# Optimization experiments

Hardware: AMD Instinct MI355X
Metric: run time of the kernel (lower is better)

## Reference

```python
import jax, jax.numpy as jnp
import numpy as np

N_NODES = 100000
N_EDGES = 1600000
DK = 32
OUT_DIM = 32


def setup_inputs() -> dict:
    key = jax.random.key(0)
    ks = jax.random.split(key, 7)
    X = jax.random.normal(ks[0], (N_NODES, DK), dtype=jnp.float32)
    K = jax.random.normal(ks[1], (N_NODES, DK), dtype=jnp.float32)
    V = jax.random.normal(ks[2], (N_NODES, DK), dtype=jnp.float32)
    # output projection (nn.Dense(out_dim)) params
    W_o = jax.random.normal(ks[3], (DK, OUT_DIM), dtype=jnp.float32) / np.sqrt(DK)
    b_o = jnp.zeros((OUT_DIM,), dtype=jnp.float32)
    # sparsity descriptor td: edge list, dst sorted so segment ops see sorted ids
    src = jax.random.randint(ks[4], (N_EDGES,), 0, N_NODES, dtype=jnp.int32)
    dst = jnp.sort(jax.random.randint(ks[5], (N_EDGES,), 0, N_NODES, dtype=jnp.int32))
    return {"X": X, "K": K, "V": V, "W_o": W_o, "b_o": b_o,
            "src": src, "dst": dst, "num_seg": N_NODES}


def reference(X, K, V, W_o, b_o, src, dst, num_seg):
    dk = X.shape[-1]
    # per-edge attention logits: <Q[dst], K[src]> / dk  -> (E,)
    scores = jnp.einsum('ed,ed->e', jnp.take(X, dst, axis=0),
                        jnp.take(K, src, axis=0)) / dk
    # segment (per-neighborhood) softmax over edges sharing a dst node
    seg_max = jax.ops.segment_max(scores, dst, num_segments=num_seg,
                                  indices_are_sorted=True)
    e = jnp.exp(scores - jnp.take(seg_max, dst))
    denom = jax.ops.segment_sum(e, dst, num_segments=num_seg,
                                indices_are_sorted=True)
    alpha = e / jnp.take(denom, dst)  # (E,)
    # weighted aggregation of values, scattered back to nodes -> (N, dk)
    agg = jax.ops.segment_sum(alpha[:, None] * jnp.take(V, src, axis=0), dst,
                              num_segments=num_seg, indices_are_sorted=True)
    # output projection W_o
    return agg @ W_o + b_o
```

## Files before the change

kernel.cpp:

```cpp
#include <hip/hip_runtime.h>
#include <math.h>

#define DK 32
#define OUT_DIM 32

typedef float    f32x4 __attribute__((ext_vector_type(4)));
typedef _Float16 h2    __attribute__((ext_vector_type(2)));
typedef _Float16 h8    __attribute__((ext_vector_type(8)));

#if __has_builtin(__builtin_amdgcn_fdot2)
#define FDOT2(a, b, c) __builtin_amdgcn_fdot2((a), (b), (c), false)
#else
#define FDOT2(a, b, c) ((c) + (float)(a).x * (float)(b).x + (float)(a).y * (float)(b).y)
#endif

#if __has_builtin(__builtin_amdgcn_exp2f)
#define EXP2F(x) __builtin_amdgcn_exp2f(x)
#else
#define EXP2F(x) exp2f(x)
#endif

__device__ __forceinline__ h2 as_h2(unsigned u) {
    union { unsigned u; h2 h; } v; v.u = u; return v.h;
}
__device__ __forceinline__ unsigned as_u32(h2 h) {
    union { unsigned u; h2 h; } v; v.h = h; return v.u;
}
__device__ __forceinline__ h2 shfl_xor_h2(h2 v, int m) {
    union { unsigned u; h2 h; } x; x.h = v;
    x.u = (unsigned)__shfl_xor((int)x.u, m);
    return x.h;
}

__global__ void prep_kernel(const int* __restrict__ dst,
                            const float4* __restrict__ K4,
                            const float4* __restrict__ V4,
                            int E, int N,
                            int* __restrict__ row_ptr,
                            uint4* __restrict__ KVH) {
    const int t  = blockIdx.x * blockDim.x + threadIdx.x;
    const int e0 = t * 4;
    if (e0 < E) {
        int cur[4];
        if (e0 + 4 <= E) {
            const int4 dd = *(const int4*)(dst + e0);
            cur[0] = dd.x; cur[1] = dd.y; cur[2] = dd.z; cur[3] = dd.w;
        } else {
#pragma unroll
            for (int k = 0; k < 4; ++k)
                cur[k] = (e0 + k < E) ? dst[e0 + k] : 0;
        }
        int prev = (e0 == 0) ? -1 : dst[e0 - 1];
#pragma unroll
        for (int k = 0; k < 4; ++k) {
            const int ee = e0 + k;
            if (ee < E) {
                for (int j = prev + 1; j <= cur[k]; ++j) row_ptr[j] = ee;
                if (ee == E - 1)
                    for (int j = cur[k] + 1; j <= N; ++j) row_ptr[j] = E;
                prev = cur[k];
            }
        }
    }
    if (t < N * 8) {
        const float4 kf = K4[t];
        const float4 vf = V4[t];
        h2 k01, k23, v01, v23;
        k01.x = (_Float16)kf.x;  k01.y = (_Float16)kf.y;
        k23.x = (_Float16)kf.z;  k23.y = (_Float16)kf.w;
        v01.x = (_Float16)vf.x;  v01.y = (_Float16)vf.y;
        v23.x = (_Float16)vf.z;  v23.y = (_Float16)vf.w;
        uint4 o;
        o.x = as_u32(k01); o.y = as_u32(k23); o.z = as_u32(v01); o.w = as_u32(v23);
        KVH[t] = o;
    }
}

__global__ void build_row_ptr_kernel(const int* __restrict__ dst, int E, int N,
                                     int* __restrict__ row_ptr) {
    int e = blockIdx.x * blockDim.x + threadIdx.x;
    if (e >= E) return;
    int cur  = dst[e];
    int prev = (e == 0) ? -1 : dst[e - 1];
    for (int j = prev + 1; j <= cur; ++j) row_ptr[j] = e;
    if (e == E - 1) {
        for (int j = cur + 1; j <= N; ++j) row_ptr[j] = E;
    }
}

__global__ __launch_bounds__(512) void gat_fused_kernel(
    const float* __restrict__ X, const uint4* __restrict__ KV,
    const float* __restrict__ Wo, const float* __restrict__ bo,
    const int* __restrict__ src, const int* __restrict__ row_ptr,
    float* __restrict__ out, int N) {

    __shared__ uint4 s_part[16 * 17];

    const int tid  = threadIdx.x;
    const int w    = tid >> 6;
    const int lane = tid & 63;
    const int g    = lane >> 3;
    const int c    = lane & 7;

    const int n_blk = blockIdx.x * 8;
    const int n     = n_blk + w;

    if (tid < 136) {
        uint4 z; z.x = 0; z.y = 0; z.z = 0; z.w = 0;
        s_part[136 + tid] = z;
    }

    const int B    = __builtin_amdgcn_readfirstlane(row_ptr[min(n, N)]);
    const int En   = __builtin_amdgcn_readfirstlane(row_ptr[min(n + 1, N)]);
    const int deg  = En - B;
    const int dcap = max(En - 1, 0);
    const int T    = (deg + 7) >> 3;

    const float scale = 0.03125f * 1.44269504f;
    const float4 qf = ((const float4*)X)[min(n, N - 1) * 8 + c];
    h2 q01, q23;
    q01.x = (_Float16)(qf.x * scale);  q01.y = (_Float16)(qf.y * scale);
    q23.x = (_Float16)(qf.z * scale);  q23.y = (_Float16)(qf.w * scale);

    float l = 0.0f;
    h2 a01 = (h2)0, a23 = (h2)0;

    auto step = [&](const uint4& Bf, int t) {
        float p = FDOT2(as_h2(Bf.y), q23, FDOT2(as_h2(Bf.x), q01, 0.0f));
        p += __shfl_xor(p, 1);
        p += __shfl_xor(p, 2);
        p += __shfl_xor(p, 4);
        const float wt = (t * 8 + g < deg) ? EXP2F(p) : 0.0f;
        l += wt;
        h2 wh; wh.x = (_Float16)wt; wh.y = wh.x;
        a01 += wh * as_h2(Bf.z);
        a23 += wh * as_h2(Bf.w);
    };

    if (T > 0) {
        const int base = B + g;
        const int s0 = src[min(base, dcap)];
        int s1 = 0, s2 = 0, s3 = 0;
        if (T > 1) s1 = src[min(base + 8,  dcap)];
        if (T > 2) s2 = src[min(base + 16, dcap)];
        if (T > 3) s3 = src[min(base + 24, dcap)];
        uint4 P0, P1, P2, P3;
        P0 = KV[s0 * 8 + c];
        if (T > 1) P1 = KV[s1 * 8 + c];
        if (T > 2) P2 = KV[s2 * 8 + c];
        if (T > 3) P3 = KV[s3 * 8 + c];

        step(P0, 0);
        if (T > 1) step(P1, 1);
        if (T > 2) step(P2, 2);
        if (T > 3) step(P3, 3);

        for (int t = 4; t < T; ++t) {
            const int sx = src[min(B + t * 8 + g, dcap)];
            const uint4 Px = KV[sx * 8 + c];
            step(Px, t);
        }
    }

    l   += __shfl_xor(l, 8);
    a01 += shfl_xor_h2(a01, 8);
    a23 += shfl_xor_h2(a23, 8);
    l += __shfl_xor(l, 16);
    l += __shfl_xor(l, 32);

    const float inv = (deg > 0) ? (1.0f / l) : 0.0f;
    h2 iv; iv.x = (_Float16)inv; iv.y = iv.x;
    a01 *= iv;  a23 *= iv;

    if ((g & 1) == 0) {
        unsigned* part32 = (unsigned*)s_part;
        const int off = w * 68 + (g >> 1) * 16 + c * 2;
        part32[off]     = as_u32(a01);
        part32[off + 1] = as_u32(a23);
    }

    __syncthreads();

    if (w == 0) {
        const int quad = lane >> 4;
        const int col  = lane & 15;

        union BF { h8 v; _Float16 u[8]; };
        BF bf0, bf1;
#pragma unroll
        for (int j2 = 0; j2 < 8; ++j2) {
            bf0.u[j2] = (_Float16)Wo[(quad * 8 + j2) * OUT_DIM + col];
            bf1.u[j2] = (_Float16)Wo[(quad * 8 + j2) * OUT_DIM + 16 + col];
        }
        const float bias0 = bo[col];
        const float bias1 = bo[16 + col];

        union AF { uint4 u; h8 v; };
        f32x4 C0 = {bias0, bias0, bias0, bias0};
        f32x4 C1 = {bias1, bias1, bias1, bias1};
#pragma unroll
        for (int cc = 0; cc < 4; ++cc) {
            AF a;
            a.u = s_part[col * 17 + cc * 4 + quad];
            C0 = __builtin_amdgcn_mfma_f32_16x16x32_f16(a.v, bf0.v, C0, 0, 0, 0);
            C1 = __builtin_amdgcn_mfma_f32_16x16x32_f16(a.v, bf1.v, C1, 0, 0, 0);
        }
        if (quad < 2) {
#pragma unroll
            for (int r = 0; r < 4; ++r) {
                const int n2 = n_blk + quad * 4 + r;
                if (n2 < N) {
                    out[n2 * OUT_DIM + col]      = C0[r];
                    out[n2 * OUT_DIM + 16 + col] = C1[r];
                }
            }
        }
    }
}

__global__ __launch_bounds__(256) void gat_node_f32_kernel(
    const float* __restrict__ X, const float* __restrict__ Km,
    const float* __restrict__ Vm, const float* __restrict__ Wo,
    const float* __restrict__ bo, const int* __restrict__ src,
    const int* __restrict__ row_ptr, float* __restrict__ out, int N) {
    const int tid  = threadIdx.x;
    const int wave = tid >> 6;
    const int lane = tid & 63;
    const int g    = lane >> 3;
    const int c    = lane & 7;
    const int j    = lane & 31;
    const int half = lane >> 5;
    const int n = blockIdx.x * 4 + wave;
    if (n >= N) return;
    const int begin = row_ptr[n];
    const int end   = row_ptr[n + 1];
    const float4* X4 = (const float4*)X;
    const float4* K4 = (const float4*)Km;
    const float4* V4 = (const float4*)Vm;
    const float4 q4 = X4[n * 8 + c];
    float  l   = 0.0f;
    float4 acc = make_float4(0.0f, 0.0f, 0.0f, 0.0f);
    for (int e0 = begin; e0 < end; e0 += 16) {
        const int  ea = e0 + g;
        const int  eb = ea + 8;
        const bool va = ea < end;
        const bool vb = eb < end;
        const int sa = src[min(ea, end - 1)];
        const int sb = src[min(eb, end - 1)];
        const float4 ka  = K4[sa * 8 + c];
        const float4 kb  = K4[sb * 8 + c];
        const float4 vva = V4[sa * 8 + c];
        const float4 vvb = V4[sb * 8 + c];
        float pa = fmaf(ka.x, q4.x, fmaf(ka.y, q4.y, fmaf(ka.z, q4.z, ka.w * q4.w)));
        float pb = fmaf(kb.x, q4.x, fmaf(kb.y, q4.y, fmaf(kb.z, q4.z, kb.w * q4.w)));
        pa += __shfl_xor(pa, 1);  pb += __shfl_xor(pb, 1);
        pa += __shfl_xor(pa, 2);  pb += __shfl_xor(pb, 2);
        pa += __shfl_xor(pa, 4);  pb += __shfl_xor(pb, 4);
        const float wa = va ? __expf(pa * 0.03125f) : 0.0f;
        const float wb = vb ? __expf(pb * 0.03125f) : 0.0f;
        l += wa + wb;
        acc.x = fmaf(wa, vva.x, acc.x);  acc.y = fmaf(wa, vva.y, acc.y);
        acc.z = fmaf(wa, vva.z, acc.z);  acc.w = fmaf(wa, vva.w, acc.w);
        acc.x = fmaf(wb, vvb.x, acc.x);  acc.y = fmaf(wb, vvb.y, acc.y);
        acc.z = fmaf(wb, vvb.z, acc.z);  acc.w = fmaf(wb, vvb.w, acc.w);
    }
#pragma unroll
    for (int m = 8; m <= 32; m <<= 1) {
        l     += __shfl_xor(l, m);
        acc.x += __shfl_xor(acc.x, m);
        acc.y += __shfl_xor(acc.y, m);
        acc.z += __shfl_xor(acc.z, m);
        acc.w += __shfl_xor(acc.w, m);
    }
    const float inv = (end > begin) ? (1.0f / l) : 0.0f;
    float ag[4] = {acc.x, acc.y, acc.z, acc.w};
    float s = 0.0f;
#pragma unroll
    for (int k = 0; k < 32; ++k) {
        const float a = __int_as_float(
            __builtin_amdgcn_readlane(__float_as_int(ag[k & 3]), k >> 2));
        s = fmaf(a, Wo[k * OUT_DIM + j], s);
    }
    if (half == 0) {
        out[n * OUT_DIM + j] = fmaf(s, inv, bo[j]);
    }
}

extern "C" void kernel_launch(void* const* d_in, const int* in_sizes, int n_in,
                              void* d_out, int out_size, void* d_ws, size_t ws_size,
                              hipStream_t stream) {
    const float* X  = (const float*)d_in[0];
    const float* Km = (const float*)d_in[1];
    const float* Vm = (const float*)d_in[2];
    const float* Wo = (const float*)d_in[3];
    const float* bo = (const float*)d_in[4];
    const int* src  = (const int*)d_in[5];
    const int* dst  = (const int*)d_in[6];

    const int N = in_sizes[0] / DK;
    const int E = in_sizes[5];

    int* row_ptr = (int*)d_ws;
    const size_t kv_off = (((size_t)(N + 1) * 4) + 127) & ~(size_t)127;
    unsigned* KV = (unsigned*)((char*)d_ws + kv_off);
    const size_t need = kv_off + (size_t)N * DK * 4;
    float* out = (float*)d_out;

    const int tb = 256;

    if (ws_size >= need) {
        const int nE4   = (E + 3) / 4;
        const int total = N * 8;
        const int prep_n = (nE4 > total) ? nE4 : total;
        prep_kernel<<<(prep_n + tb - 1) / tb, tb, 0, stream>>>(
            dst, (const float4*)Km, (const float4*)Vm, E, N,
            row_ptr, (uint4*)KV);
        const int grid = (N + 7) / 8;
        gat_fused_kernel<<<grid, 512, 0, stream>>>(X, (const uint4*)KV, Wo, bo,
                                                   src, row_ptr, out, N);
    } else {
        build_row_ptr_kernel<<<(E + tb - 1) / tb, tb, 0, stream>>>(dst, E, N, row_ptr);
        const int grid = (N + 3) / 4;
        gat_node_f32_kernel<<<grid, 256, 0, stream>>>(X, Km, Vm, Wo, bo,
                                                      src, row_ptr, out, N);
    }
}
```

Before: 141.6 us.

## Quantize K/V rows to int8 with per-row scales for edge gather

The prep kernel now quantizes each K and V row to symmetric int8 with a per-row fp16 scale, interleaving K and V bytes so each lane fetches 8 bytes per edge instead of 16. The fused kernel dequantizes on the fly and accumulates the weighted values in fp32 rather than packed fp16. This halves the bytes moved by the random src gather and adds one extra scale load per edge. It also adds integer unpacking ALU work and int8 quantization error in the scores and values.

After: 146.4 us. +3.4%, slower.

```diff
diff --git a/kernel.cpp b/kernel.cpp
--- a/kernel.cpp
+++ b/kernel.cpp
@@ -7,12 +7,6 @@
 typedef float    f32x4 __attribute__((ext_vector_type(4)));
 typedef _Float16 h2    __attribute__((ext_vector_type(2)));
 typedef _Float16 h8    __attribute__((ext_vector_type(8)));
-
-#if __has_builtin(__builtin_amdgcn_fdot2)
-#define FDOT2(a, b, c) __builtin_amdgcn_fdot2((a), (b), (c), false)
-#else
-#define FDOT2(a, b, c) ((c) + (float)(a).x * (float)(b).x + (float)(a).y * (float)(b).y)
-#endif
 
 #if __has_builtin(__builtin_amdgcn_exp2f)
 #define EXP2F(x) __builtin_amdgcn_exp2f(x)
@@ -26,10 +20,15 @@
 __device__ __forceinline__ unsigned as_u32(h2 h) {
     union { unsigned u; h2 h; } v; v.h = h; return v.u;
 }
-__device__ __forceinline__ h2 shfl_xor_h2(h2 v, int m) {
-    union { unsigned u; h2 h; } x; x.h = v;
-    x.u = (unsigned)__shfl_xor((int)x.u, m);
-    return x.h;
+
+__device__ __forceinline__ unsigned q8b(float x, float r) {
+    int i = (int)rintf(x * r);
+    i = min(127, max(-127, i));
+    return (unsigned)(i & 255);
+}
+__device__ __forceinline__ unsigned pack8x4(float4 f, float r) {
+    return q8b(f.x, r) | (q8b(f.y, r) << 8) |
+           (q8b(f.z, r) << 16) | (q8b(f.w, r) << 24);
 }
 
 __global__ void prep_kernel(const int* __restrict__ dst,
@@ -37,7 +36,8 @@
                             const float4* __restrict__ V4,
                             int E, int N,
                             int* __restrict__ row_ptr,
-                            uint4* __restrict__ KVH) {
+                            uint2* __restrict__ ROW,
+                            unsigned* __restrict__ SC) {
     const int t  = blockIdx.x * blockDim.x + threadIdx.x;
     const int e0 = t * 4;
     if (e0 < E) {
@@ -62,17 +62,34 @@
             }
         }
     }
-    if (t < N * 8) {
-        const float4 kf = K4[t];
-        const float4 vf = V4[t];
-        h2 k01, k23, v01, v23;
-        k01.x = (_Float16)kf.x;  k01.y = (_Float16)kf.y;
-        k23.x = (_Float16)kf.z;  k23.y = (_Float16)kf.w;
-        v01.x = (_Float16)vf.x;  v01.y = (_Float16)vf.y;
-        v23.x = (_Float16)vf.z;  v23.y = (_Float16)vf.w;
-        uint4 o;
-        o.x = as_u32(k01); o.y = as_u32(k23); o.z = as_u32(v01); o.w = as_u32(v23);
-        KVH[t] = o;
+    if (t < N) {
+        float4 kf[8], vf[8];
+#pragma unroll
+        for (int u = 0; u < 8; ++u) { kf[u] = K4[t * 8 + u]; vf[u] = V4[t * 8 + u]; }
+        float mk = 0.0f, mv = 0.0f;
+#pragma unroll
+        for (int u = 0; u < 8; ++u) {
+            mk = fmaxf(mk, fmaxf(fmaxf(fabsf(kf[u].x), fabsf(kf[u].y)),
+                                 fmaxf(fabsf(kf[u].z), fabsf(kf[u].w))));
+            mv = fmaxf(mv, fmaxf(fmaxf(fabsf(vf[u].x), fabsf(vf[u].y)),
+                                 fmaxf(fabsf(vf[u].z), fabsf(vf[u].w))));
+        }
+        const float rk = (mk > 0.0f) ? 127.0f / mk : 0.0f;
+        const float rv = (mv > 0.0f) ? 127.0f / mv : 0.0f;
+        uint4* o4 = (uint4*)(ROW + t * 8);
+#pragma unroll
+        for (int u2 = 0; u2 < 4; ++u2) {
+            uint4 o;
+            o.x = pack8x4(kf[2 * u2],     rk);
+            o.y = pack8x4(vf[2 * u2],     rv);
+            o.z = pack8x4(kf[2 * u2 + 1], rk);
+            o.w = pack8x4(vf[2 * u2 + 1], rv);
+            o4[u2] = o;
+        }
+        h2 s;
+        s.x = (_Float16)(mk * (1.0f / 127.0f));
+        s.y = (_Float16)(mv * (1.0f / 127.0f));
+        SC[t] = as_u32(s);
     }
 }
 
@@ -89,7 +106,8 @@
 }
 
 __global__ __launch_bounds__(512) void gat_fused_kernel(
-    const float* __restrict__ X, const uint4* __restrict__ KV,
+    const float* __restrict__ X, const uint2* __restrict__ ROW,
+    const unsigned* __restrict__ SC,
     const float* __restrict__ Wo, const float* __restrict__ bo,
     const int* __restrict__ src, const int* __restrict__ row_ptr,
     float* __restrict__ out, int N) {
@@ -117,24 +135,37 @@
     const int T    = (deg + 7) >> 3;
 
     const float scale = 0.03125f * 1.44269504f;
-    const float4 qf = ((const float4*)X)[min(n, N - 1) * 8 + c];
-    h2 q01, q23;
-    q01.x = (_Float16)(qf.x * scale);  q01.y = (_Float16)(qf.y * scale);
-    q23.x = (_Float16)(qf.z * scale);  q23.y = (_Float16)(qf.w * scale);
+    float4 qf = ((const float4*)X)[min(n, N - 1) * 8 + c];
+    qf.x *= scale; qf.y *= scale; qf.z *= scale; qf.w *= scale;
 
     float l = 0.0f;
-    h2 a01 = (h2)0, a23 = (h2)0;
-
-    auto step = [&](const uint4& Bf, int t) {
-        float p = FDOT2(as_h2(Bf.y), q23, FDOT2(as_h2(Bf.x), q01, 0.0f));
+    f32x4 acc = {0.0f, 0.0f, 0.0f, 0.0f};
+
+    auto step = [&](uint2 rv, unsigned sc, int t) {
+        const h2 sch = as_h2(sc);
+        const float sK = (float)sch.x;
+        const float sV = (float)sch.y;
+        const int b0 = (int)(char)(rv.x);
+        const int b1 = (int)(char)(rv.x >> 8);
+        const int b2 = (int)(char)(rv.x >> 16);
+        const int b3 = (int)(char)(rv.x >> 24);
+        float p = fmaf(qf.x, (float)b0, fmaf(qf.y, (float)b1,
+                  fmaf(qf.z, (float)b2, qf.w * (float)b3)));
         p += __shfl_xor(p, 1);
         p += __shfl_xor(p, 2);
         p += __shfl_xor(p, 4);
+        p *= sK;
         const float wt = (t * 8 + g < deg) ? EXP2F(p) : 0.0f;
         l += wt;
-        h2 wh; wh.x = (_Float16)wt; wh.y = wh.x;
-        a01 += wh * as_h2(Bf.z);
-        a23 += wh * as_h2(Bf.w);
+        const float wv = wt * sV;
+        const int c0 = (int)(char)(rv.y);
+        const int c1 = (int)(char)(rv.y >> 8);
+        const int c2 = (int)(char)(rv.y >> 16);
+        const int c3 = (int)(char)(rv.y >> 24);
+        acc.x = fmaf(wv, (float)c0, acc.x);
+        acc.y = fmaf(wv, (float)c1, acc.y);
+        acc.z = fmaf(wv, (float)c2, acc.z);
+        acc.w = fmaf(wv, (float)c3, acc.w);
     };
 
     if (T > 0) {
@@ -144,39 +175,42 @@
         if (T > 1) s1 = src[min(base + 8,  dcap)];
         if (T > 2) s2 = src[min(base + 16, dcap)];
         if (T > 3) s3 = src[min(base + 24, dcap)];
-        uint4 P0, P1, P2, P3;
-        P0 = KV[s0 * 8 + c];
-        if (T > 1) P1 = KV[s1 * 8 + c];
-        if (T > 2) P2 = KV[s2 * 8 + c];
-        if (T > 3) P3 = KV[s3 * 8 + c];
-
-        step(P0, 0);
-        if (T > 1) step(P1, 1);
-        if (T > 2) step(P2, 2);
-        if (T > 3) step(P3, 3);
+        uint2 r0 = {0, 0}, r1 = {0, 0}, r2 = {0, 0}, r3 = {0, 0};
+        unsigned x0 = 0, x1 = 0, x2 = 0, x3 = 0;
+        r0 = ROW[s0 * 8 + c];               x0 = SC[s0];
+        if (T > 1) { r1 = ROW[s1 * 8 + c];  x1 = SC[s1]; }
+        if (T > 2) { r2 = ROW[s2 * 8 + c];  x2 = SC[s2]; }
+        if (T > 3) { r3 = ROW[s3 * 8 + c];  x3 = SC[s3]; }
+
+        step(r0, x0, 0);
+        if (T > 1) step(r1, x1, 1);
+        if (T > 2) step(r2, x2, 2);
+        if (T > 3) step(r3, x3, 3);
 
         for (int t = 4; t < T; ++t) {
             const int sx = src[min(B + t * 8 + g, dcap)];
-            const uint4 Px = KV[sx * 8 + c];
-            step(Px, t);
-        }
-    }
-
-    l   += __shfl_xor(l, 8);
-    a01 += shfl_xor_h2(a01, 8);
-    a23 += shfl_xor_h2(a23, 8);
+            step(ROW[sx * 8 + c], SC[sx], t);
+        }
+    }
+
+    l     += __shfl_xor(l, 8);
+    acc.x += __shfl_xor(acc.x, 8);
+    acc.y += __shfl_xor(acc.y, 8);
+    acc.z += __shfl_xor(acc.z, 8);
+    acc.w += __shfl_xor(acc.w, 8);
     l += __shfl_xor(l, 16);
     l += __shfl_xor(l, 32);
 
     const float inv = (deg > 0) ? (1.0f / l) : 0.0f;
-    h2 iv; iv.x = (_Float16)inv; iv.y = iv.x;
-    a01 *= iv;  a23 *= iv;
+    h2 o01, o23;
+    o01.x = (_Float16)(acc.x * inv);  o01.y = (_Float16)(acc.y * inv);
+    o23.x = (_Float16)(acc.z * inv);  o23.y = (_Float16)(acc.w * inv);
 
     if ((g & 1) == 0) {
         unsigned* part32 = (unsigned*)s_part;
         const int off = w * 68 + (g >> 1) * 16 + c * 2;
-        part32[off]     = as_u32(a01);
-        part32[off + 1] = as_u32(a23);
+        part32[off]     = as_u32(o01);
+        part32[off + 1] = as_u32(o23);
     }
 
     __syncthreads();
@@ -301,22 +335,23 @@
     const int E = in_sizes[5];
 
     int* row_ptr = (int*)d_ws;
-    const size_t kv_off = (((size_t)(N + 1) * 4) + 127) & ~(size_t)127;
-    unsigned* KV = (unsigned*)((char*)d_ws + kv_off);
-    const size_t need = kv_off + (size_t)N * DK * 4;
+    const size_t row_off = (((size_t)(N + 1) * 4) + 127) & ~(size_t)127;
+    const size_t sc_off  = ((row_off + (size_t)N * 64) + 127) & ~(size_t)127;
+    uint2*    ROW = (uint2*)((char*)d_ws + row_off);
+    unsigned* SCt = (unsigned*)((char*)d_ws + sc_off);
+    const size_t need = sc_off + (size_t)N * 4;
     float* out = (float*)d_out;
 
     const int tb = 256;
 
     if (ws_size >= need) {
         const int nE4   = (E + 3) / 4;
-        const int total = N * 8;
-        const int prep_n = (nE4 > total) ? nE4 : total;
+        const int prep_n = (nE4 > N) ? nE4 : N;
         prep_kernel<<<(prep_n + tb - 1) / tb, tb, 0, stream>>>(
             dst, (const float4*)Km, (const float4*)Vm, E, N,
-            row_ptr, (uint4*)KV);
+            row_ptr, ROW, SCt);
         const int grid = (N + 7) / 8;
-        gat_fused_kernel<<<grid, 512, 0, stream>>>(X, (const uint4*)KV, Wo, bo,
+        gat_fused_kernel<<<grid, 512, 0, stream>>>(X, ROW, SCt, Wo, bo,
                                                    src, row_ptr, out, N);
     } else {
         build_row_ptr_kernel<<<(E + tb - 1) / tb, tb, 0, stream>>>(dst, E, N, row_ptr);
```
